# Kernel optimization log

Hardware: AMD Instinct MI355X
Metric: run time of the kernel (lower is better)

The kernel has to match this reference:

```python
import jax, jax.numpy as jnp
import numpy as np

D_MODEL, D_STATE, D_CONV, EXPAND = 512, 16, 4, 2
D_INNER = EXPAND * D_MODEL
DT_RANK = -(-D_MODEL // 16)  # ceil(512/16) = 32
B, L = 1, 2048


def setup_inputs() -> dict:
    key = jax.random.key(0)
    ks = jax.random.split(key, 10)
    x = jax.random.normal(ks[0], (B, L, D_MODEL), dtype=jnp.float32)
    in_proj_w = jax.random.normal(ks[1], (2 * D_INNER, D_MODEL), dtype=jnp.float32) * (D_MODEL ** -0.5)
    conv_w = jax.random.normal(ks[2], (D_INNER, 1, D_CONV), dtype=jnp.float32) * (D_CONV ** -0.5)
    conv_b = jax.random.normal(ks[3], (D_INNER,), dtype=jnp.float32) * 0.02
    x_proj_w = jax.random.normal(ks[4], (DT_RANK + 2 * D_STATE, D_INNER), dtype=jnp.float32) * (D_INNER ** -0.5)
    dt_init_std = DT_RANK ** -0.5
    dt_proj_w = jax.random.uniform(ks[5], (D_INNER, DT_RANK), minval=-dt_init_std, maxval=dt_init_std, dtype=jnp.float32)
    # dt bias init: inverse-softplus of dt sampled log-uniform in [dt_min, dt_max]
    dt = jnp.exp(jax.random.uniform(ks[6], (D_INNER,)) * (np.log(0.1) - np.log(0.001)) + np.log(0.001))
    dt = jnp.clip(dt, 1e-4, None)
    dt_proj_b = dt + jnp.log(-jnp.expm1(-dt))
    A_log = jnp.log(jnp.broadcast_to(jnp.arange(1, D_STATE + 1, dtype=jnp.float32), (D_INNER, D_STATE)))
    D = jnp.ones((D_INNER,), dtype=jnp.float32)
    out_proj_w = jax.random.normal(ks[7], (D_MODEL, D_INNER), dtype=jnp.float32) * (D_INNER ** -0.5)
    return {"x": x, "in_proj_w": in_proj_w, "conv_w": conv_w, "conv_b": conv_b,
            "x_proj_w": x_proj_w, "dt_proj_w": dt_proj_w, "dt_proj_b": dt_proj_b,
            "A_log": A_log, "D": D, "out_proj_w": out_proj_w}


def _selective_scan_parallel(x, deltaA, deltaB, C):
    # x: (B,L,D)  deltaA/deltaB: (B,L,D,N)  C: (B,L,N)
    log_dA = jnp.log(jnp.clip(deltaA, 1e-6, None))
    cum_dA = jnp.exp(jnp.cumsum(log_dA, axis=1))                      # (B,L,D,N)
    Bx = deltaB * x[..., None]                                        # (B,L,D,N)
    cum_dA_prev = jnp.concatenate([jnp.ones_like(cum_dA[:, :1]), cum_dA[:, :-1]], axis=1)
    h = cum_dA * jnp.cumsum(Bx / (cum_dA_prev + 1e-8), axis=1)        # (B,L,D,N)
    return jnp.einsum('bldn,bln->bld', h, C)


def reference(x, in_proj_w, conv_w, conv_b, x_proj_w, dt_proj_w, dt_proj_b, A_log, D, out_proj_w):
    xz = jnp.einsum('bld,ed->ble', x, in_proj_w)            # (B,L,2*D_inner)
    xp, z = jnp.split(xz, 2, axis=-1)
    # causal depthwise conv1d: left-pad d_conv-1, groups = d_inner
    xc = jax.lax.conv_general_dilated(
        jnp.transpose(xp, (0, 2, 1)), conv_w, window_strides=(1,),
        padding=[(D_CONV - 1, 0)], dimension_numbers=('NCH', 'OIH', 'NCH'),
        feature_group_count=D_INNER) + conv_b[None, :, None]
    xp = jax.nn.silu(jnp.transpose(xc, (0, 2, 1)))          # (B,L,D_inner)
    # SSM
    A = -jnp.exp(A_log.astype(jnp.float32))                 # (D_inner, N)
    x_dbl = jnp.einsum('bld,ed->ble', xp, x_proj_w)
    delta, Bm, Cm = jnp.split(x_dbl, [DT_RANK, DT_RANK + D_STATE], axis=-1)
    delta = jax.nn.softplus(jnp.einsum('blr,dr->bld', delta, dt_proj_w) + dt_proj_b)
    deltaA = jnp.exp(delta[..., None] * A)                  # (B,L,D,N)
    deltaB = delta[..., None] * Bm[:, :, None, :]           # (B,L,D,N)
    y = _selective_scan_parallel(xp, deltaA, deltaB, Cm)
    y = y + xp * D
    out = y * jax.nn.silu(z)
    return jnp.einsum('bld,md->blm', out, out_proj_w)
```

## Files before the change

kernel.cpp:

```cpp
#include <hip/hip_runtime.h>
#include <hip/hip_bf16.h>

#define L_SEQ   2048
#define D_MODEL 512
#define D_INNER 1024
#define D_STATE 16
#define DT_RANK 32

typedef unsigned short u16;
typedef short bf16x8 __attribute__((ext_vector_type(8)));
typedef float f32x4  __attribute__((ext_vector_type(4)));
typedef unsigned short u16x8 __attribute__((ext_vector_type(8)));

__device__ __forceinline__ u16 f2bf(float f) {
    union { float f; unsigned u; } x; x.f = f;
    unsigned r = x.u + 0x7FFFu + ((x.u >> 16) & 1u);
    return (u16)(r >> 16);
}

__device__ __forceinline__ void gload_lds16(const void* g, void* l) {
    __builtin_amdgcn_global_load_lds((const __attribute__((address_space(1))) void*)g,
                                     (__attribute__((address_space(3))) void*)l, 16, 0, 0);
}

template<int BM, int BN>
__global__ __launch_bounds__(256)
void gemm_mfma_nt(const u16* __restrict__ A, const u16* __restrict__ B,
                  float* __restrict__ C, int M, int N, int K, int ldc) {
    constexpr int FM = BM / 32;
    constexpr int FN = BN / 32;
    __shared__ u16 lA[BM * 64];
    __shared__ u16 lB[BN * 64];

    const int tid  = threadIdx.x;
    const int lane = tid & 63;
    const int w    = tid >> 6;
    const int wr   = w >> 1, wc = w & 1;
    const int m0 = blockIdx.y * BM;
    const int n0 = blockIdx.x * BN;

    f32x4 acc[FM][FN];
#pragma unroll
    for (int m = 0; m < FM; m++)
#pragma unroll
        for (int n = 0; n < FN; n++) acc[m][n] = (f32x4){0.f, 0.f, 0.f, 0.f};

    int offA[FM][2], offB[FN][2];
#pragma unroll
    for (int m = 0; m < FM; m++) {
        int r = wr * (BM / 2) + m * 16 + (lane & 15);
#pragma unroll
        for (int s = 0; s < 2; s++) {
            int kb = s * 4 + (lane >> 4);
            offA[m][s] = r * 128 + ((kb ^ (r & 7)) << 4);
        }
    }
#pragma unroll
    for (int n = 0; n < FN; n++) {
        int r = wc * (BN / 2) + n * 16 + (lane & 15);
#pragma unroll
        for (int s = 0; s < 2; s++) {
            int kb = s * 4 + (lane >> 4);
            offB[n][s] = r * 128 + ((kb ^ (r & 7)) << 4);
        }
    }

    const int ldsbase = (tid & 192) * 16;

    for (int k0 = 0; k0 < K; k0 += 64) {
        __syncthreads();
#pragma unroll
        for (int i = 0; i < BM / 32; i++) {
            int o = i * 4096 + tid * 16;
            int r = o >> 7;
            int kb = ((o >> 4) & 7) ^ (r & 7);
            gload_lds16(A + (size_t)(m0 + r) * K + k0 + kb * 8,
                        (char*)lA + i * 4096 + ldsbase);
        }
#pragma unroll
        for (int i = 0; i < BN / 32; i++) {
            int o = i * 4096 + tid * 16;
            int r = o >> 7;
            int kb = ((o >> 4) & 7) ^ (r & 7);
            gload_lds16(B + (size_t)(n0 + r) * K + k0 + kb * 8,
                        (char*)lB + i * 4096 + ldsbase);
        }
        __syncthreads();

#pragma unroll
        for (int s = 0; s < 2; s++) {
            bf16x8 av[FM], bv[FN];
#pragma unroll
            for (int m = 0; m < FM; m++)
                av[m] = *(const bf16x8*)((const char*)lA + offA[m][s]);
#pragma unroll
            for (int n = 0; n < FN; n++)
                bv[n] = *(const bf16x8*)((const char*)lB + offB[n][s]);
#pragma unroll
            for (int m = 0; m < FM; m++)
#pragma unroll
                for (int n = 0; n < FN; n++)
                    acc[m][n] = __builtin_amdgcn_mfma_f32_16x16x32_bf16(
                        av[m], bv[n], acc[m][n], 0, 0, 0);
        }
    }

    const int rb = (lane >> 4) * 4;
    const int cb = lane & 15;
#pragma unroll
    for (int m = 0; m < FM; m++)
#pragma unroll
        for (int n = 0; n < FN; n++) {
            int col = n0 + wc * (BN / 2) + n * 16 + cb;
#pragma unroll
            for (int j = 0; j < 4; j++) {
                int row = m0 + wr * (BM / 2) + m * 16 + rb + j;
                C[(size_t)row * ldc + col] = acc[m][n][j];
            }
        }
}

__global__ __launch_bounds__(256)
void cast3_kernel(const float* __restrict__ x, const float* __restrict__ w1,
                  const float* __restrict__ w2,
                  u16* __restrict__ xb, u16* __restrict__ w1b, u16* __restrict__ w2b) {
    int g = blockIdx.x * 256 + threadIdx.x;
    const float* src; u16* dst; int off;
    if (g < 131072)      { src = x;  dst = xb;  off = g; }
    else if (g < 262144) { src = w1; dst = w1b; off = g - 131072; }
    else                 { src = w2; dst = w2b; off = g - 262144; }
    float4 v0 = ((const float4*)src)[off * 2];
    float4 v1 = ((const float4*)src)[off * 2 + 1];
    u16x8 r;
    r[0] = f2bf(v0.x); r[1] = f2bf(v0.y); r[2] = f2bf(v0.z); r[3] = f2bf(v0.w);
    r[4] = f2bf(v1.x); r[5] = f2bf(v1.y); r[6] = f2bf(v1.z); r[7] = f2bf(v1.w);
    *(u16x8*)(dst + (size_t)off * 8) = r;
}

__global__ __launch_bounds__(256)
void conv_rows_kernel(const float* __restrict__ xzT,
                      const float* __restrict__ w,
                      const float* __restrict__ b,
                      float* __restrict__ xpcT) {
    const int d = blockIdx.y;
    const int l = blockIdx.x * 1024 + threadIdx.x * 4;
    const float4 wv = ((const float4*)w)[d];
    const float bias = b[d];
    const float* row = xzT + (size_t)d * L_SEQ;

    float4 cur  = *(const float4*)(row + l);
    float4 prev = (l == 0) ? make_float4(0.f, 0.f, 0.f, 0.f)
                           : *(const float4*)(row + l - 4);
    float e1 = prev.y, e2 = prev.z, e3 = prev.w;
    float e4 = cur.x, e5 = cur.y, e6 = cur.z, e7 = cur.w;
    float4 r;
    r.x = bias + wv.x * e1 + wv.y * e2 + wv.z * e3 + wv.w * e4;
    r.y = bias + wv.x * e2 + wv.y * e3 + wv.z * e4 + wv.w * e5;
    r.z = bias + wv.x * e3 + wv.y * e4 + wv.z * e5 + wv.w * e6;
    r.w = bias + wv.x * e4 + wv.y * e5 + wv.z * e6 + wv.w * e7;
    r.x = r.x / (1.f + __expf(-r.x));
    r.y = r.y / (1.f + __expf(-r.y));
    r.z = r.z / (1.f + __expf(-r.z));
    r.w = r.w / (1.f + __expf(-r.w));
    *(float4*)(xpcT + (size_t)d * L_SEQ + l) = r;
}

__global__ __launch_bounds__(256)
void xproj_kernel(const float* __restrict__ xpcT,
                  const float* __restrict__ xw,
                  float* __restrict__ xdblT) {
    const int tid  = threadIdx.x;
    const int part = tid >> 7;
    const int e    = (tid >> 1) & 63;
    const int lc   = tid & 1;
    const int l0   = blockIdx.x * 8;

    const float* wrow = xw + (size_t)e * 1024 + part * 512;
    const float* xcol = xpcT + (size_t)part * 512 * L_SEQ + l0 + lc * 4;

    f32x4 acc = {0.f, 0.f, 0.f, 0.f};
#pragma unroll 4
    for (int k = 0; k < 512; k += 4) {
        float4 wv = *(const float4*)(wrow + k);
        f32x4 x0 = *(const f32x4*)(xcol + (size_t)(k + 0) * L_SEQ);
        f32x4 x1 = *(const f32x4*)(xcol + (size_t)(k + 1) * L_SEQ);
        f32x4 x2 = *(const f32x4*)(xcol + (size_t)(k + 2) * L_SEQ);
        f32x4 x3 = *(const f32x4*)(xcol + (size_t)(k + 3) * L_SEQ);
        acc += wv.x * x0 + wv.y * x1 + wv.z * x2 + wv.w * x3;
    }

    __shared__ f32x4 red[128];
    if (part == 1) red[(e << 1) | lc] = acc;
    __syncthreads();
    if (part == 0) {
        acc += red[(e << 1) | lc];
        *(f32x4*)(xdblT + (size_t)e * L_SEQ + l0 + lc * 4) = acc;
    }
}

__global__ __launch_bounds__(256)
void deltaT_kernel(const float* __restrict__ xdblT,
                   const float* __restrict__ dtw,
                   const float* __restrict__ dtb,
                   float* __restrict__ deltaT) {
    const int tid = threadIdx.x;
    const int d0 = blockIdx.x * 64;
    const int l0 = blockIdx.y * 128;

    __shared__ float sx[32][128];
#pragma unroll
    for (int it = 0; it < 4; it++) {
        int idx = it * 256 + tid;
        int r  = idx >> 5;
        int c4 = (idx & 31) * 4;
        *(float4*)&sx[r][c4] = *(const float4*)(xdblT + (size_t)r * 2048 + l0 + c4);
    }

    const int dl = tid >> 2;
    const int lg = tid & 3;
    const int d  = d0 + dl;
    float wreg[32];
#pragma unroll
    for (int r4 = 0; r4 < 32; r4 += 4)
        *(float4*)&wreg[r4] = *(const float4*)(dtw + (size_t)d * 32 + r4);
    const float bias = dtb[d];
    __syncthreads();

#pragma unroll
    for (int j = 0; j < 8; j++) {
        float4 a = make_float4(bias, bias, bias, bias);
        const int col = j * 16 + lg * 4;
#pragma unroll
        for (int r = 0; r < 32; r++) {
            float4 v = *(const float4*)&sx[r][col];
            a.x = fmaf(wreg[r], v.x, a.x);
            a.y = fmaf(wreg[r], v.y, a.y);
            a.z = fmaf(wreg[r], v.z, a.z);
            a.w = fmaf(wreg[r], v.w, a.w);
        }
        float4 o;
        o.x = fmaxf(a.x, 0.f) + log1pf(expf(-fabsf(a.x)));
        o.y = fmaxf(a.y, 0.f) + log1pf(expf(-fabsf(a.y)));
        o.z = fmaxf(a.z, 0.f) + log1pf(expf(-fabsf(a.z)));
        o.w = fmaxf(a.w, 0.f) + log1pf(expf(-fabsf(a.w)));
        *(float4*)(deltaT + (size_t)d * 2048 + l0 + col) = o;
    }
}

#define NCHUNK 32

__global__ __launch_bounds__(1024)
void scan_kernel(const float* __restrict__ deltaT,
                 const float* __restrict__ xpcT,
                 const float* __restrict__ xzT,
                 const float* __restrict__ xdblT,
                 const float* __restrict__ A_log, const float* __restrict__ Dv,
                 u16* __restrict__ ypreT) {
    const int tid   = threadIdx.x;
    const int lane  = tid & 63;
    const int chunk = ((tid >> 6) << 1) | (lane >> 5);
    const int dl    = (lane >> 4) & 1;
    const int n     = lane & 15;
    const int li    = (dl << 4) | n;
    const int d0    = blockIdx.x * 2;
    const int d     = d0 + dl;
    const int lb    = chunk * 64;

    const float Aneg = -__expf(A_log[d * D_STATE + n]);
    const float Dd   = Dv[d];

    const f32x4* dT4 = (const f32x4*)(deltaT + (size_t)d * L_SEQ + lb);
    const f32x4* xT4 = (const f32x4*)(xpcT   + (size_t)d * L_SEQ + lb);
    const f32x4* zT4 = (const f32x4*)(xzT    + (size_t)(1024 + d) * L_SEQ + lb);
    const f32x4* bT4 = (const f32x4*)(xdblT + (size_t)(32 + n) * L_SEQ + lb);
    const f32x4* cT4 = (const f32x4*)(xdblT + (size_t)(48 + n) * L_SEQ + lb);

    __shared__ float sLog[NCHUNK][32];
    __shared__ float sP[NCHUNK][32];
    __shared__ float sH[NCHUNK][32];
    __shared__ float s_y[2][L_SEQ];

    const float clipLog = -13.815511f;
    float s = 0.f;
#pragma unroll 8
    for (int i = 0; i < 16; i++) {
        f32x4 d4 = dT4[i];
#pragma unroll
        for (int k = 0; k < 4; k++) s += fmaxf(d4[k] * Aneg, clipLog);
    }
    sLog[chunk][li] = s;
    sP[chunk][li]   = __expf(s);
    __syncthreads();

    float lsum = 0.f;
    for (int v = 0; v < chunk; v++) lsum += sLog[v][li];
    const float cAs = __expf(lsum);

    float hloc = 0.f, cA = cAs;
    for (int i = 0; i < 16; i++) {
        f32x4 d4 = dT4[i], x4 = xT4[i], b4 = bT4[i];
#pragma unroll
        for (int k = 0; k < 4; k++) {
            float dA = fmaxf(__expf(d4[k] * Aneg), 1e-6f);
            float g  = cA * __builtin_amdgcn_rcpf(cA + 1e-8f);
            hloc = dA * hloc + (dA * g) * (d4[k] * b4[k] * x4[k]);
            cA *= dA;
        }
    }
    sH[chunk][li] = hloc;
    __syncthreads();

    float h = 0.f;
    for (int v = 0; v < chunk; v++) h = sP[v][li] * h + sH[v][li];

    cA = cAs;
    for (int i = 0; i < 16; i++) {
        f32x4 d4 = dT4[i], x4 = xT4[i], b4 = bT4[i], c4 = cT4[i];
        f32x4 z4 = zT4[i];
#pragma unroll
        for (int k = 0; k < 4; k++) {
            float dA = fmaxf(__expf(d4[k] * Aneg), 1e-6f);
            float g  = cA * __builtin_amdgcn_rcpf(cA + 1e-8f);
            h  = dA * h + (dA * g) * (d4[k] * b4[k] * x4[k]);
            cA *= dA;
            float p = h * c4[k];
            p += __shfl_xor(p, 1);
            p += __shfl_xor(p, 2);
            p += __shfl_xor(p, 4);
            p += __shfl_xor(p, 8);
            if (n == 0) {
                float sz = z4[k] * __builtin_amdgcn_rcpf(1.f + __expf(-z4[k]));
                s_y[dl][lb + 4 * i + k] = (p + x4[k] * Dd) * sz;
            }
        }
    }
    __syncthreads();

    {
        const int rdl = tid >> 9;
        const int pos = (tid & 511) * 4;
        f32x4 v = *(const f32x4*)&s_y[rdl][pos];
        ushort4 o;
        o.x = f2bf(v[0]); o.y = f2bf(v[1]); o.z = f2bf(v[2]); o.w = f2bf(v[3]);
        *(ushort4*)(ypreT + (size_t)(d0 + rdl) * L_SEQ + pos) = o;
    }
}

__global__ __launch_bounds__(256)
void trans_bf16_kernel(const u16* __restrict__ src, u16* __restrict__ dst) {
    __shared__ u16 t[64][72];
    const int d0 = blockIdx.x * 64, l0 = blockIdx.y * 64;
    const int r = threadIdx.x >> 3;
    const int c = (threadIdx.x & 7) * 8;
#pragma unroll
    for (int rr = r; rr < 64; rr += 32)
        *(u16x8*)&t[rr][c] = *(const u16x8*)(src + (size_t)(d0 + rr) * L_SEQ + l0 + c);
    __syncthreads();
#pragma unroll
    for (int rr = r; rr < 64; rr += 32) {
        u16x8 v;
#pragma unroll
        for (int j = 0; j < 8; j++) v[j] = t[c + j][rr];
        *(u16x8*)(dst + (size_t)(l0 + rr) * D_INNER + d0 + c) = v;
    }
}

extern "C" void kernel_launch(void* const* d_in, const int* in_sizes, int n_in,
                              void* d_out, int out_size, void* d_ws, size_t ws_size,
                              hipStream_t stream) {
    const float* x          = (const float*)d_in[0];
    const float* in_proj_w  = (const float*)d_in[1];
    const float* conv_w     = (const float*)d_in[2];
    const float* conv_b     = (const float*)d_in[3];
    const float* x_proj_w   = (const float*)d_in[4];
    const float* dt_proj_w  = (const float*)d_in[5];
    const float* dt_proj_b  = (const float*)d_in[6];
    const float* A_log      = (const float*)d_in[7];
    const float* Dv         = (const float*)d_in[8];
    const float* out_proj_w = (const float*)d_in[9];
    float* out = (float*)d_out;
    float* ws  = (float*)d_ws;

    float* xzT    = ws;
    float* xpcT   = ws + 4194304;
    float* xdblT  = ws + 6291456;
    float* deltaT = ws + 6422528;
    u16*   ypreT  = (u16*)(ws + 8519680);
    u16*   ypre   = (u16*)(ws + 9568256);
    u16*   xb     = (u16*)(ws + 10616832);
    u16*   w1b    = (u16*)(ws + 11141120);
    u16*   w2b    = (u16*)(ws + 11665408);

    cast3_kernel<<<1280, 256, 0, stream>>>(x, in_proj_w, out_proj_w, xb, w1b, w2b);

    gemm_mfma_nt<64, 64><<<dim3(2048 / 64, 2048 / 64), 256, 0, stream>>>(
        w1b, xb, xzT, 2 * D_INNER, L_SEQ, D_MODEL, L_SEQ);

    conv_rows_kernel<<<dim3(2, 1024), 256, 0, stream>>>(xzT, conv_w, conv_b, xpcT);

    xproj_kernel<<<256, 256, 0, stream>>>(xpcT, x_proj_w, xdblT);

    deltaT_kernel<<<dim3(16, 16), 256, 0, stream>>>(xdblT, dt_proj_w, dt_proj_b,
                                                    deltaT);

    scan_kernel<<<512, 1024, 0, stream>>>(deltaT, xpcT, xzT, xdblT,
                                          A_log, Dv, ypreT);

    trans_bf16_kernel<<<dim3(16, 32), 256, 0, stream>>>(ypreT, ypre);

    gemm_mfma_nt<64, 32><<<dim3(512 / 32, 2048 / 64), 256, 0, stream>>>(
        ypre, w2b, out, L_SEQ, D_MODEL, D_INNER, D_MODEL);
}
```

Measured before the change: 158.4 us.

## Scan one channel per block and move gating epilogue out of scan loop

```diff
diff --git a/kernel.cpp b/kernel.cpp
--- a/kernel.cpp
+++ b/kernel.cpp
@@ -249,7 +249,7 @@
 
 #define NCHUNK 32
 
-__global__ __launch_bounds__(1024)
+__global__ __launch_bounds__(512)
 void scan_kernel(const float* __restrict__ deltaT,
                  const float* __restrict__ xpcT,
                  const float* __restrict__ xzT,
@@ -258,12 +258,9 @@
                  u16* __restrict__ ypreT) {
     const int tid   = threadIdx.x;
     const int lane  = tid & 63;
-    const int chunk = ((tid >> 6) << 1) | (lane >> 5);
-    const int dl    = (lane >> 4) & 1;
+    const int chunk = ((tid >> 6) << 2) | (lane >> 4);
     const int n     = lane & 15;
-    const int li    = (dl << 4) | n;
-    const int d0    = blockIdx.x * 2;
-    const int d     = d0 + dl;
+    const int d     = blockIdx.x;
     const int lb    = chunk * 64;
 
     const float Aneg = -__expf(A_log[d * D_STATE + n]);
@@ -271,14 +268,13 @@
 
     const f32x4* dT4 = (const f32x4*)(deltaT + (size_t)d * L_SEQ + lb);
     const f32x4* xT4 = (const f32x4*)(xpcT   + (size_t)d * L_SEQ + lb);
-    const f32x4* zT4 = (const f32x4*)(xzT    + (size_t)(1024 + d) * L_SEQ + lb);
     const f32x4* bT4 = (const f32x4*)(xdblT + (size_t)(32 + n) * L_SEQ + lb);
     const f32x4* cT4 = (const f32x4*)(xdblT + (size_t)(48 + n) * L_SEQ + lb);
 
-    __shared__ float sLog[NCHUNK][32];
-    __shared__ float sP[NCHUNK][32];
-    __shared__ float sH[NCHUNK][32];
-    __shared__ float s_y[2][L_SEQ];
+    __shared__ float sLog[NCHUNK][17];
+    __shared__ float sP[NCHUNK][17];
+    __shared__ float sH[NCHUNK][17];
+    __shared__ float s_p[NCHUNK][68];
 
     const float clipLog = -13.815511f;
     float s = 0.f;
@@ -288,12 +284,12 @@
 #pragma unroll
         for (int k = 0; k < 4; k++) s += fmaxf(d4[k] * Aneg, clipLog);
     }
-    sLog[chunk][li] = s;
-    sP[chunk][li]   = __expf(s);
+    sLog[chunk][n] = s;
+    sP[chunk][n]   = __expf(s);
     __syncthreads();
 
     float lsum = 0.f;
-    for (int v = 0; v < chunk; v++) lsum += sLog[v][li];
+    for (int v = 0; v < chunk; v++) lsum += sLog[v][n];
     const float cAs = __expf(lsum);
 
     float hloc = 0.f, cA = cAs;
@@ -307,16 +303,15 @@
             cA *= dA;
         }
     }
-    sH[chunk][li] = hloc;
+    sH[chunk][n] = hloc;
     __syncthreads();
 
     float h = 0.f;
-    for (int v = 0; v < chunk; v++) h = sP[v][li] * h + sH[v][li];
+    for (int v = 0; v < chunk; v++) h = sP[v][n] * h + sH[v][n];
 
     cA = cAs;
     for (int i = 0; i < 16; i++) {
         f32x4 d4 = dT4[i], x4 = xT4[i], b4 = bT4[i], c4 = cT4[i];
-        f32x4 z4 = zT4[i];
 #pragma unroll
         for (int k = 0; k < 4; k++) {
             float dA = fmaxf(__expf(d4[k] * Aneg), 1e-6f);
@@ -328,21 +323,24 @@
             p += __shfl_xor(p, 2);
             p += __shfl_xor(p, 4);
             p += __shfl_xor(p, 8);
-            if (n == 0) {
-                float sz = z4[k] * __builtin_amdgcn_rcpf(1.f + __expf(-z4[k]));
-                s_y[dl][lb + 4 * i + k] = (p + x4[k] * Dd) * sz;
-            }
+            if (n == 0) s_p[chunk][4 * i + k] = p;
         }
     }
     __syncthreads();
 
     {
-        const int rdl = tid >> 9;
-        const int pos = (tid & 511) * 4;
-        f32x4 v = *(const f32x4*)&s_y[rdl][pos];
+        const int l0 = tid * 4;
+        const int ck = l0 >> 6, off = l0 & 63;
+        f32x4 p4 = *(const f32x4*)&s_p[ck][off];
+        f32x4 x4 = *(const f32x4*)(xpcT + (size_t)d * L_SEQ + l0);
+        f32x4 z4 = *(const f32x4*)(xzT + (size_t)(1024 + d) * L_SEQ + l0);
         ushort4 o;
-        o.x = f2bf(v[0]); o.y = f2bf(v[1]); o.z = f2bf(v[2]); o.w = f2bf(v[3]);
-        *(ushort4*)(ypreT + (size_t)(d0 + rdl) * L_SEQ + pos) = o;
+        float y0 = (p4[0] + x4[0] * Dd) * (z4[0] * __builtin_amdgcn_rcpf(1.f + __expf(-z4[0])));
+        float y1 = (p4[1] + x4[1] * Dd) * (z4[1] * __builtin_amdgcn_rcpf(1.f + __expf(-z4[1])));
+        float y2 = (p4[2] + x4[2] * Dd) * (z4[2] * __builtin_amdgcn_rcpf(1.f + __expf(-z4[2])));
+        float y3 = (p4[3] + x4[3] * Dd) * (z4[3] * __builtin_amdgcn_rcpf(1.f + __expf(-z4[3])));
+        o.x = f2bf(y0); o.y = f2bf(y1); o.z = f2bf(y2); o.w = f2bf(y3);
+        *(ushort4*)(ypreT + (size_t)d * L_SEQ + l0) = o;
     }
 }
 
@@ -403,7 +401,7 @@
     deltaT_kernel<<<dim3(16, 16), 256, 0, stream>>>(xdblT, dt_proj_w, dt_proj_b,
                                                     deltaT);
 
-    scan_kernel<<<512, 1024, 0, stream>>>(deltaT, xpcT, xzT, xdblT,
+    scan_kernel<<<1024, 512, 0, stream>>>(deltaT, xpcT, xzT, xdblT,
                                           A_log, Dv, ypreT);
 
     trans_bf16_kernel<<<dim3(16, 32), 256, 0, stream>>>(ypreT, ypre);
```

Result: slower. 186.8 us (+17.9%).
